# Optimization experiments

Measured on AMD Instinct MI355X. Metric: run time of the kernel, lower is better.

Reference implementation:

```python
import jax, jax.numpy as jnp
import numpy as np

B, S, HID = 1, 4096, 1024
HQ, HKV, D = 16, 4, 64   # query heads, kv heads (GQA), dim_per_head
ROPE_BASE = 10000.0


def setup_inputs() -> dict:
    key = jax.random.key(0)
    ks = jax.random.split(key, 5)
    s = 0.02
    return {
        "x": jax.random.normal(ks[0], (B, S, HID), jnp.float32),
        "Wq": jax.random.normal(ks[1], (HID, HQ * D), jnp.float32) * s,
        "Wk": jax.random.normal(ks[2], (HID, HKV * D), jnp.float32) * s,
        "Wv": jax.random.normal(ks[3], (HID, HKV * D), jnp.float32) * s,
        "Wo": jax.random.normal(ks[4], (HQ * D, HID), jnp.float32) * s,
    }


def _rope(t, cos, sin):
    # non-interleaved (half-split) rotary; t: [B,S,H,D], cos/sin: [S, D//2]
    t1, t2 = jnp.split(t, 2, axis=-1)
    c = cos[None, :, None, :]
    sn = sin[None, :, None, :]
    return jnp.concatenate([t1 * c - t2 * sn, t2 * c + t1 * sn], axis=-1)


def reference(x, Wq, Wk, Wv, Wo):
    # QKV projections (self-attention: key=value=query=x), reshape to [B,S,H,D]
    q = (x @ Wq).reshape(B, S, HQ, D)
    k = (x @ Wk).reshape(B, S, HKV, D)
    v = (x @ Wv).reshape(B, S, HKV, D)

    # rotary position embedding over full head dim
    inv_freq = 1.0 / (ROPE_BASE ** (jnp.arange(0, D, 2, dtype=jnp.float32) / D))
    ang = jnp.arange(S, dtype=jnp.float32)[:, None] * inv_freq[None, :]  # [S, D//2]
    cos, sin = jnp.cos(ang), jnp.sin(ang)
    q = _rope(q, cos, sin)
    k = _rope(k, cos, sin)

    # GQA: expand kv heads to match query heads
    g = HQ // HKV
    k = jnp.repeat(k, g, axis=2)
    v = jnp.repeat(v, g, axis=2)

    scale = D ** -0.5  # attn_scaling ** -0.5 with attn_scaling = dim_per_head
    scores = jnp.einsum('bqhd,bkhd->bhqk', q, k) * scale  # [B,HQ,S,S]
    causal = jnp.tril(jnp.ones((S, S), dtype=bool))
    scores = jnp.where(causal[None, None], scores, jnp.finfo(scores.dtype).min)
    attn = jax.nn.softmax(scores, axis=-1)

    ctx = jnp.einsum('bhqk,bkhd->bqhd', attn, v).reshape(B, S, HQ * D)
    return ctx @ Wo
```

## Files before the change

### kernel.cpp

```cpp
#include <hip/hip_runtime.h>
#include <hip/hip_bf16.h>
#include <math.h>

typedef __attribute__((ext_vector_type(8))) short short8;
typedef __attribute__((ext_vector_type(4))) float f32x4;

#define S_   4096
#define HQ_  16
#define HKV_ 4
#define D_   64

static __device__ __forceinline__ unsigned short f2b(float f) {
    __hip_bfloat16 h = __float2bfloat16(f);
    return *reinterpret_cast<unsigned short*>(&h);
}
static __device__ __forceinline__ float b2f(unsigned short u) {
    union { unsigned int u; float f; } c;
    c.u = ((unsigned int)u) << 16;
    return c.f;
}

typedef __attribute__((address_space(1))) const unsigned int gas_u32;
typedef __attribute__((address_space(3))) unsigned int las_u32;
static __device__ __forceinline__ void gload16(const void* g, void* l) {
    __builtin_amdgcn_global_load_lds((gas_u32*)g, (las_u32*)l, 16, 0, 0);
}


__global__ __launch_bounds__(256) void k_prep(const float* __restrict__ Wq,
                                              const float* __restrict__ Wk,
                                              const float* __restrict__ Wv,
                                              const float* __restrict__ Wo,
                                              const float* __restrict__ x,
                                              unsigned short* __restrict__ WT,
                                              unsigned short* __restrict__ WoT,
                                              unsigned short* __restrict__ xb,
                                              float* __restrict__ cs) {
    const int z = blockIdx.z;
    const int t = threadIdx.x;
    if (z == 4) {
        int flat = blockIdx.y * 32 + blockIdx.x;
#pragma unroll
        for (int ii = 0; ii < 4; ++ii) {
            int i = flat * 1024 + ii * 256 + t;
            float4 v = ((const float4*)x)[i];
            ushort4 o;
            o.x = f2b(v.x); o.y = f2b(v.y); o.z = f2b(v.z); o.w = f2b(v.w);
            ((ushort4*)xb)[i] = o;
        }
        return;
    }
    if (z == 5) {
        int flat = blockIdx.y * 32 + blockIdx.x;
        if (flat >= 512) return;
        int i = flat * 256 + t;
        int s = i >> 5, jj = i & 31;
        float invf = exp2f(-(float)jj * (13.287712379549449f / 32.0f));
        float ang = (float)s * invf;
        ((float2*)cs)[i] = make_float2(cosf(ang), sinf(ang));
        return;
    }
    const float* tin; unsigned short* tout; int N, gx;
    if (z == 0)      { tin = Wq; tout = WT;                 N = 1024; gx = 32; }
    else if (z == 1) { tin = Wk; tout = WT + 1024 * 1024;   N = 256;  gx = 8;  }
    else if (z == 2) { tin = Wv; tout = WT + 1280 * 1024;   N = 256;  gx = 8;  }
    else             { tin = Wo; tout = WoT;                N = 1024; gx = 32; }
    if ((int)blockIdx.x >= gx) return;
    __shared__ float tile[32][33];
    int tx = t & 31, ty = t >> 5;
    int n0 = blockIdx.x * 32, k0 = blockIdx.y * 32;
#pragma unroll
    for (int r = 0; r < 32; r += 8)
        tile[ty + r][tx] = tin[(size_t)(k0 + ty + r) * N + n0 + tx];
    __syncthreads();
#pragma unroll
    for (int r = 0; r < 32; r += 8)
        tout[(size_t)(n0 + ty + r) * 1024 + k0 + tx] = f2b(tile[tx][ty + r]);
}


__global__ __launch_bounds__(256, 3)
void k_gemm_qkv(const unsigned short* __restrict__ A,
                const unsigned short* __restrict__ BT,
                const float* __restrict__ cs,
                unsigned short* __restrict__ Qr,
                unsigned short* __restrict__ Kr,
                unsigned short* __restrict__ Vt) {
    __shared__ unsigned short As[128 * 128];
    __shared__ unsigned short Bs[64 * 128];
    const int t = threadIdx.x;
    const int ntile = blockIdx.x;
    const int n0 = ntile * 64;
    const int m0 = blockIdx.y * 128;
    const int w = t >> 6, lane = t & 63, lr = lane & 15, lg = lane >> 4;
    const int srr = w * 4 + (lane >> 4);
    const int sby = (lane & 15) * 16;
    const int K = 1024;

    f32x4 acc[2][4];
#pragma unroll
    for (int m = 0; m < 2; ++m)
#pragma unroll
        for (int n = 0; n < 4; ++n) acc[m][n] = (f32x4){0.f, 0.f, 0.f, 0.f};

    for (int k0 = 0; k0 < K; k0 += 128) {
#pragma unroll
        for (int c = 0; c < 8; ++c) {
            int r = c * 16 + srr;
            gload16((const char*)&A[(size_t)(m0 + r) * K + k0] + (sby ^ ((r & 7) << 4)),
                    (char*)As + c * 4096 + w * 1024);
        }
#pragma unroll
        for (int c = 0; c < 4; ++c) {
            int r = c * 16 + srr;
            gload16((const char*)&BT[(size_t)(n0 + r) * K + k0] + (sby ^ ((r & 7) << 4)),
                    (char*)Bs + c * 4096 + w * 1024);
        }
        __syncthreads();
#pragma unroll
        for (int kk = 0; kk < 4; ++kk) {
            short8 af[2], bf[4];
#pragma unroll
            for (int m = 0; m < 2; ++m) {
                int arow = w * 32 + m * 16 + lr;
                af[m] = *(const short8*)((const char*)As + arow * 256 +
                                         ((kk * 64 + lg * 16) ^ ((arow & 7) << 4)));
            }
#pragma unroll
            for (int n = 0; n < 4; ++n) {
                int brow = n * 16 + lr;
                bf[n] = *(const short8*)((const char*)Bs + brow * 256 +
                                         ((kk * 64 + lg * 16) ^ ((brow & 7) << 4)));
            }
#pragma unroll
            for (int m = 0; m < 2; ++m)
#pragma unroll
                for (int n = 0; n < 4; ++n)
                    acc[m][n] = __builtin_amdgcn_mfma_f32_16x16x32_bf16(af[m], bf[n], acc[m][n], 0, 0, 0);
        }
        __syncthreads();
    }

    if (ntile < 20) {
        const float QS = (ntile < 16) ? 0.125f * 1.44269504088896340736f : 1.0f;
        unsigned short* dst = (ntile < 16) ? (Qr + (size_t)ntile * (S_ * D_))
                                           : (Kr + (size_t)(ntile - 16) * (S_ * D_));
#pragma unroll
        for (int m = 0; m < 2; ++m)
#pragma unroll
            for (int rr = 0; rr < 4; ++rr) {
                int s = m0 + w * 32 + m * 16 + lg * 4 + rr;
                const float2* csr = (const float2*)cs + s * 32;
                float2 c0 = csr[lr];
                float2 c1 = csr[16 + lr];
                float t1 = acc[m][0][rr], t2 = acc[m][2][rr];
                dst[(size_t)s * 64 + lr]      = f2b((t1 * c0.x - t2 * c0.y) * QS);
                dst[(size_t)s * 64 + 32 + lr] = f2b((t2 * c0.x + t1 * c0.y) * QS);
                t1 = acc[m][1][rr]; t2 = acc[m][3][rr];
                dst[(size_t)s * 64 + 16 + lr] = f2b((t1 * c1.x - t2 * c1.y) * QS);
                dst[(size_t)s * 64 + 48 + lr] = f2b((t2 * c1.x + t1 * c1.y) * QS);
            }
    } else {
        int h2 = ntile - 20;
        unsigned short* dst = Vt + (size_t)h2 * (D_ * S_);
#pragma unroll
        for (int m = 0; m < 2; ++m)
#pragma unroll
            for (int n = 0; n < 4; ++n)
#pragma unroll
                for (int rr = 0; rr < 4; ++rr) {
                    int s = m0 + w * 32 + m * 16 + lg * 4 + rr;
                    dst[(size_t)(n * 16 + lr) * S_ + s] = f2b(acc[m][n][rr]);
                }
    }
}


__global__ __launch_bounds__(256, 3)
void k_gemm_o(const unsigned short* __restrict__ A,
              const unsigned short* __restrict__ BT,
              float* __restrict__ out) {
    __shared__ unsigned short As[128 * 128];
    __shared__ unsigned short Bs[64 * 128];
    const int t = threadIdx.x;
    const int n0 = blockIdx.x * 64;
    const int m0 = blockIdx.y * 128;
    const int w = t >> 6, lane = t & 63, lr = lane & 15, lg = lane >> 4;
    const int srr = w * 4 + (lane >> 4);
    const int sby = (lane & 15) * 16;
    const int K = 1024;

    f32x4 acc[2][4];
#pragma unroll
    for (int m = 0; m < 2; ++m)
#pragma unroll
        for (int n = 0; n < 4; ++n) acc[m][n] = (f32x4){0.f, 0.f, 0.f, 0.f};

    for (int k0 = 0; k0 < K; k0 += 128) {
#pragma unroll
        for (int c = 0; c < 8; ++c) {
            int r = c * 16 + srr;
            gload16((const char*)&A[(size_t)(m0 + r) * K + k0] + (sby ^ ((r & 7) << 4)),
                    (char*)As + c * 4096 + w * 1024);
        }
#pragma unroll
        for (int c = 0; c < 4; ++c) {
            int r = c * 16 + srr;
            gload16((const char*)&BT[(size_t)(n0 + r) * K + k0] + (sby ^ ((r & 7) << 4)),
                    (char*)Bs + c * 4096 + w * 1024);
        }
        __syncthreads();
#pragma unroll
        for (int kk = 0; kk < 4; ++kk) {
            short8 af[2], bf[4];
#pragma unroll
            for (int m = 0; m < 2; ++m) {
                int arow = w * 32 + m * 16 + lr;
                af[m] = *(const short8*)((const char*)As + arow * 256 +
                                         ((kk * 64 + lg * 16) ^ ((arow & 7) << 4)));
            }
#pragma unroll
            for (int n = 0; n < 4; ++n) {
                int brow = n * 16 + lr;
                bf[n] = *(const short8*)((const char*)Bs + brow * 256 +
                                         ((kk * 64 + lg * 16) ^ ((brow & 7) << 4)));
            }
#pragma unroll
            for (int m = 0; m < 2; ++m)
#pragma unroll
                for (int n = 0; n < 4; ++n)
                    acc[m][n] = __builtin_amdgcn_mfma_f32_16x16x32_bf16(af[m], bf[n], acc[m][n], 0, 0, 0);
        }
        __syncthreads();
    }
#pragma unroll
    for (int m = 0; m < 2; ++m)
#pragma unroll
        for (int n = 0; n < 4; ++n)
#pragma unroll
            for (int rr = 0; rr < 4; ++rr) {
                int row = m0 + w * 32 + m * 16 + lg * 4 + rr;
                int col = n0 + n * 16 + lr;
                out[(size_t)row * 1024 + col] = acc[m][n][rr];
            }
}


__global__ __launch_bounds__(256, 4)
void k_attn(const unsigned short* __restrict__ Qr,
            const unsigned short* __restrict__ Kr,
            const unsigned short* __restrict__ Vt,
            unsigned short* __restrict__ Pacc,
            float* __restrict__ Psv) {
    __shared__ unsigned short Ks[2][64 * 64];
    __shared__ unsigned short Vs[2][64 * 64];

    const int t = threadIdx.x;
    const int p = blockIdx.x;
    const int h = blockIdx.y;
    const int j = blockIdx.z;
    const int kvh = h >> 2;
    const int w = t >> 6, lane = t & 63, lr = lane & 15, lg = lane >> 4;

    const unsigned short* Qh = Qr + (size_t)h * (S_ * D_);
    const unsigned short* Kh = Kr + (size_t)kvh * (S_ * D_);
    const unsigned short* Vh = Vt + (size_t)kvh * (D_ * S_);

    const int xw = (lr & 7) << 4;
    const int sr = lane >> 3, sch = (lane & 7) * 16;
    const int r0a = w * 16, r0b = w * 16 + 8;

#pragma unroll 1
    for (int half = 0; half < 2; ++half) {
        const int qb = half ? p : (63 - p);
        const int tend = qb + 1;
        const int qi = qb * 64 + w * 16 + lr;

        const char* kp[2];
        const char* vp[2];
        {
            int ra = r0a + sr, rb = r0b + sr;
            kp[0] = (const char*)(Kh + (size_t)(j * 64 + ra) * 64) + (sch ^ ((ra & 7) << 4));
            kp[1] = (const char*)(Kh + (size_t)(j * 64 + rb) * 64) + (sch ^ ((rb & 7) << 4));
            vp[0] = (const char*)(Vh + (size_t)ra * S_ + j * 64) + (sch ^ ((ra & 7) << 4));
            vp[1] = (const char*)(Vh + (size_t)rb * S_ + j * 64) + (sch ^ ((rb & 7) << 4));
        }
        auto stage = [&](int buf) {
            gload16(kp[0], (char*)&Ks[buf][0] + r0a * 128);
            gload16(kp[1], (char*)&Ks[buf][0] + r0b * 128);
            gload16(vp[0], (char*)&Vs[buf][0] + r0a * 128);
            gload16(vp[1], (char*)&Vs[buf][0] + r0b * 128);
            kp[0] += 16384; kp[1] += 16384;
            vp[0] += 256;   vp[1] += 256;
        };

        short8 aq[2];
        {
            int qrow = qb * 64 + w * 16 + lr;
            aq[0] = *(const short8*)&Qh[(size_t)qrow * 64 + lg * 8];
            aq[1] = *(const short8*)&Qh[(size_t)qrow * 64 + 32 + lg * 8];
        }
        float svl = 0.f;
        f32x4 acc_o[4];
#pragma unroll
        for (int i = 0; i < 4; ++i) acc_o[i] = (f32x4){0.f, 0.f, 0.f, 0.f};

        int cur = 0;
        stage(0);
        __syncthreads();

        for (int kb = j; kb < tend; kb += 2) {
            if (kb + 2 < tend) stage(cur ^ 1);

            f32x4 s[4];
#pragma unroll
            for (int i = 0; i < 4; ++i) s[i] = (f32x4){0.f, 0.f, 0.f, 0.f};
            const char* KsB = (const char*)&Ks[cur][0];
            __builtin_amdgcn_s_setprio(1);
#pragma unroll
            for (int kk = 0; kk < 2; ++kk)
#pragma unroll
                for (int nt = 0; nt < 4; ++nt) {
                    int brow = nt * 16 + lr;
                    short8 kf = *(const short8*)(KsB + brow * 128 + ((kk * 64 + lg * 16) ^ xw));
                    s[nt] = __builtin_amdgcn_mfma_f32_16x16x32_bf16(kf, aq[kk], s[nt], 0, 0, 0);
                }
            __builtin_amdgcn_s_setprio(0);

            if (kb == qb) {
                int kbase = kb * 64 + lg * 4;
#pragma unroll
                for (int nt = 0; nt < 4; ++nt)
#pragma unroll
                    for (int rr = 0; rr < 4; ++rr)
                        if (kbase + nt * 16 + rr > qi) s[nt][rr] = -INFINITY;
            }

            unsigned int wd[8];
#pragma unroll
            for (int nt = 0; nt < 4; ++nt) {
                float p0 = exp2f(s[nt][0]), p1 = exp2f(s[nt][1]);
                float p2 = exp2f(s[nt][2]), p3 = exp2f(s[nt][3]);
                svl += (p0 + p1) + (p2 + p3);
                asm("v_cvt_pk_bf16_f32 %0, %1, %2" : "=v"(wd[nt * 2])     : "v"(p0), "v"(p1));
                asm("v_cvt_pk_bf16_f32 %0, %1, %2" : "=v"(wd[nt * 2 + 1]) : "v"(p2), "v"(p3));
            }

            const char* VsB = (const char*)&Vs[cur][0];
            __builtin_amdgcn_s_setprio(1);
#pragma unroll
            for (int kk = 0; kk < 2; ++kk) {
                union { unsigned int u[4]; short8 s8; } pa;
                pa.u[0] = wd[4 * kk + 0]; pa.u[1] = wd[4 * kk + 1];
                pa.u[2] = wd[4 * kk + 2]; pa.u[3] = wd[4 * kk + 3];
#pragma unroll
                for (int nt = 0; nt < 4; ++nt) {
                    int drow = nt * 16 + lr;
                    union { unsigned long long q[2]; short8 s8; } vb;
                    vb.q[0] = *(const unsigned long long*)(VsB + drow * 128 +
                              ((kk * 64 + lg * 8) ^ xw));
                    vb.q[1] = *(const unsigned long long*)(VsB + drow * 128 +
                              ((kk * 64 + 32 + lg * 8) ^ xw));
                    acc_o[nt] = __builtin_amdgcn_mfma_f32_16x16x32_bf16(pa.s8, vb.s8, acc_o[nt], 0, 0, 0);
                }
            }
            __builtin_amdgcn_s_setprio(0);

            __syncthreads();
            cur ^= 1;
        }

        svl += __shfl_xor(svl, 16);
        svl += __shfl_xor(svl, 32);
        const int u = ((j * 64 + qb) * 16 + h);
        if (lg == 0) Psv[u * 64 + w * 16 + lr] = svl;
        unsigned short* Pb = Pacc + (size_t)u * 4096;
#pragma unroll
        for (int nt = 0; nt < 4; ++nt) {
            int rr = w * 16 + lg * 4;
            int col = nt * 16 + lr;
            Pb[(rr + 0) * 64 + col] = f2b(acc_o[nt][0]);
            Pb[(rr + 1) * 64 + col] = f2b(acc_o[nt][1]);
            Pb[(rr + 2) * 64 + col] = f2b(acc_o[nt][2]);
            Pb[(rr + 3) * 64 + col] = f2b(acc_o[nt][3]);
        }
    }
}


__global__ __launch_bounds__(256) void k_combine(const unsigned short* __restrict__ Pacc,
                                                 const float* __restrict__ Psv,
                                                 unsigned short* __restrict__ O) {
    const int qb = blockIdx.x, h = blockIdx.y;
    const int t = threadIdx.x;
    const int r = t >> 2, db = (t & 3) * 16;
    const int u0 = (qb * 16 + h);
    const int u1 = ((64 + qb) * 16 + h);
    float sa = Psv[u0 * 64 + r], sb = Psv[u1 * 64 + r];
    float inv = 1.f / (sa + sb);
    const unsigned short* A_ = Pacc + (size_t)u0 * 4096 + r * 64 + db;
    const unsigned short* B_ = Pacc + (size_t)u1 * 4096 + r * 64 + db;
    unsigned short* Op = O + (size_t)(qb * 64 + r) * 1024 + h * 64 + db;
#pragma unroll
    for (int halfv = 0; halfv < 2; ++halfv) {
        short8 va = *(const short8*)(A_ + halfv * 8);
        short8 vb = *(const short8*)(B_ + halfv * 8);
        short8 o;
#pragma unroll
        for (int i = 0; i < 8; ++i)
            o[i] = (short)f2b((b2f((unsigned short)va[i]) + b2f((unsigned short)vb[i])) * inv);
        *(short8*)(Op + halfv * 8) = o;
    }
}


extern "C" void kernel_launch(void* const* d_in, const int* in_sizes, int n_in,
                              void* d_out, int out_size, void* d_ws, size_t ws_size,
                              hipStream_t stream) {
    const float* x  = (const float*)d_in[0];
    const float* Wq = (const float*)d_in[1];
    const float* Wk = (const float*)d_in[2];
    const float* Wv = (const float*)d_in[3];
    const float* Wo = (const float*)d_in[4];
    float* out = (float*)d_out;
    char* ws = (char*)d_ws;

    unsigned short* WT  = (unsigned short*)(ws + 0);
    unsigned short* WoT = (unsigned short*)(ws + 3145728);
    unsigned short* Qr  = (unsigned short*)(ws + 5242880);
    unsigned short* Kr  = (unsigned short*)(ws + 13631488);
    unsigned short* Vt  = (unsigned short*)(ws + 15728640);
    unsigned short* O   = (unsigned short*)(ws + 17825792);
    float* cs           = (float*)(ws + 26214400);
    unsigned short* xb  = (unsigned short*)(ws + 27262976);
    unsigned short* Pacc = (unsigned short*)(ws + 27262976);
    float* Psv           = (float*)(ws + 44040192);

    k_prep<<<dim3(32, 32, 6), 256, 0, stream>>>(Wq, Wk, Wv, Wo, x, WT, WoT, xb, cs);
    k_gemm_qkv<<<dim3(24, 32), 256, 0, stream>>>(xb, WT, cs, Qr, Kr, Vt);
    k_attn<<<dim3(32, 16, 2), 256, 0, stream>>>(Qr, Kr, Vt, Pacc, Psv);
    k_combine<<<dim3(64, 16), 256, 0, stream>>>(Pacc, Psv, O);
    k_gemm_o<<<dim3(16, 32), 256, 0, stream>>>(O, WoT, out);
}
```

Measured before the change: 120.6 us.

## Process 128 query rows per attention block and permute V layout for vector loads

The attention kernel now handles a 128-row query tile per block, with each wave owning two 16-row MFMA fragments. Each K/V tile staged in shared memory therefore feeds twice as many MFMAs, and the earlier two-half load-balancing loop is replaced by reverse block ordering. The V store in the QKV GEMM writes a permuted position order as 4-wide vector stores, so the attention PV step can read V fragments with a single 16-byte load instead of two 8-byte loads. This costs more registers per wave, which may lower occupancy under the four-blocks launch bound, and it coarsens the causal-diagonal work per block.

```diff
diff --git a/kernel.cpp b/kernel.cpp
--- a/kernel.cpp
+++ b/kernel.cpp
@@ -85,7 +85,7 @@
                 const float* __restrict__ cs,
                 unsigned short* __restrict__ Qr,
                 unsigned short* __restrict__ Kr,
-                unsigned short* __restrict__ Vt) {
+                unsigned short* __restrict__ Vp) {
     __shared__ unsigned short As[128 * 128];
     __shared__ unsigned short Bs[64 * 128];
     const int t = threadIdx.x;
@@ -162,16 +162,18 @@
             }
     } else {
         int h2 = ntile - 20;
-        unsigned short* dst = Vt + (size_t)h2 * (D_ * S_);
+        unsigned short* dst = Vp + (size_t)h2 * (D_ * S_);
 #pragma unroll
         for (int m = 0; m < 2; ++m)
 #pragma unroll
-            for (int n = 0; n < 4; ++n)
-#pragma unroll
-                for (int rr = 0; rr < 4; ++rr) {
-                    int s = m0 + w * 32 + m * 16 + lg * 4 + rr;
-                    dst[(size_t)(n * 16 + lr) * S_ + s] = f2b(acc[m][n][rr]);
-                }
+            for (int n = 0; n < 4; ++n) {
+                int d = n * 16 + lr;
+                int pos = m0 + (w >> 1) * 64 + (w & 1) * 32 + lg * 8 + m * 4;
+                ushort4 o;
+                o.x = f2b(acc[m][n][0]); o.y = f2b(acc[m][n][1]);
+                o.z = f2b(acc[m][n][2]); o.w = f2b(acc[m][n][3]);
+                *(ushort4*)&dst[(size_t)d * S_ + pos] = o;
+            }
     }
 }
 
@@ -249,14 +251,14 @@
 __global__ __launch_bounds__(256, 4)
 void k_attn(const unsigned short* __restrict__ Qr,
             const unsigned short* __restrict__ Kr,
-            const unsigned short* __restrict__ Vt,
+            const unsigned short* __restrict__ Vp,
             unsigned short* __restrict__ Pacc,
             float* __restrict__ Psv) {
     __shared__ unsigned short Ks[2][64 * 64];
     __shared__ unsigned short Vs[2][64 * 64];
 
     const int t = threadIdx.x;
-    const int p = blockIdx.x;
+    const int qb = 31 - (int)blockIdx.x;
     const int h = blockIdx.y;
     const int j = blockIdx.z;
     const int kvh = h >> 2;
@@ -264,143 +266,152 @@
 
     const unsigned short* Qh = Qr + (size_t)h * (S_ * D_);
     const unsigned short* Kh = Kr + (size_t)kvh * (S_ * D_);
-    const unsigned short* Vh = Vt + (size_t)kvh * (D_ * S_);
+    const unsigned short* Vh = Vp + (size_t)kvh * (D_ * S_);
 
     const int xw = (lr & 7) << 4;
     const int sr = lane >> 3, sch = (lane & 7) * 16;
     const int r0a = w * 16, r0b = w * 16 + 8;
 
-#pragma unroll 1
-    for (int half = 0; half < 2; ++half) {
-        const int qb = half ? p : (63 - p);
-        const int tend = qb + 1;
-        const int qi = qb * 64 + w * 16 + lr;
-
-        const char* kp[2];
-        const char* vp[2];
-        {
-            int ra = r0a + sr, rb = r0b + sr;
-            kp[0] = (const char*)(Kh + (size_t)(j * 64 + ra) * 64) + (sch ^ ((ra & 7) << 4));
-            kp[1] = (const char*)(Kh + (size_t)(j * 64 + rb) * 64) + (sch ^ ((rb & 7) << 4));
-            vp[0] = (const char*)(Vh + (size_t)ra * S_ + j * 64) + (sch ^ ((ra & 7) << 4));
-            vp[1] = (const char*)(Vh + (size_t)rb * S_ + j * 64) + (sch ^ ((rb & 7) << 4));
-        }
-        auto stage = [&](int buf) {
-            gload16(kp[0], (char*)&Ks[buf][0] + r0a * 128);
-            gload16(kp[1], (char*)&Ks[buf][0] + r0b * 128);
-            gload16(vp[0], (char*)&Vs[buf][0] + r0a * 128);
-            gload16(vp[1], (char*)&Vs[buf][0] + r0b * 128);
-            kp[0] += 16384; kp[1] += 16384;
-            vp[0] += 256;   vp[1] += 256;
-        };
-
-        short8 aq[2];
-        {
-            int qrow = qb * 64 + w * 16 + lr;
-            aq[0] = *(const short8*)&Qh[(size_t)qrow * 64 + lg * 8];
-            aq[1] = *(const short8*)&Qh[(size_t)qrow * 64 + 32 + lg * 8];
-        }
-        float svl = 0.f;
-        f32x4 acc_o[4];
-#pragma unroll
-        for (int i = 0; i < 4; ++i) acc_o[i] = (f32x4){0.f, 0.f, 0.f, 0.f};
-
-        int cur = 0;
-        stage(0);
+    const char* kp[2];
+    const char* vp[2];
+    {
+        int ra = r0a + sr, rb = r0b + sr;
+        kp[0] = (const char*)(Kh + (size_t)(j * 64 + ra) * 64) + (sch ^ ((ra & 7) << 4));
+        kp[1] = (const char*)(Kh + (size_t)(j * 64 + rb) * 64) + (sch ^ ((rb & 7) << 4));
+        vp[0] = (const char*)(Vh + (size_t)ra * S_ + j * 64) + (sch ^ ((ra & 7) << 4));
+        vp[1] = (const char*)(Vh + (size_t)rb * S_ + j * 64) + (sch ^ ((rb & 7) << 4));
+    }
+    auto stage = [&](int buf) {
+        gload16(kp[0], (char*)&Ks[buf][0] + r0a * 128);
+        gload16(kp[1], (char*)&Ks[buf][0] + r0b * 128);
+        gload16(vp[0], (char*)&Vs[buf][0] + r0a * 128);
+        gload16(vp[1], (char*)&Vs[buf][0] + r0b * 128);
+        kp[0] += 16384; kp[1] += 16384;
+        vp[0] += 256;   vp[1] += 256;
+    };
+
+    const int qi0 = qb * 128 + w * 32 + lr;
+    short8 aq0[2], aq1[2];
+    {
+        int q0 = qi0;
+        aq0[0] = *(const short8*)&Qh[(size_t)q0 * 64 + lg * 8];
+        aq0[1] = *(const short8*)&Qh[(size_t)q0 * 64 + 32 + lg * 8];
+        aq1[0] = *(const short8*)&Qh[(size_t)(q0 + 16) * 64 + lg * 8];
+        aq1[1] = *(const short8*)&Qh[(size_t)(q0 + 16) * 64 + 32 + lg * 8];
+    }
+    float svl0 = 0.f, svl1 = 0.f;
+    f32x4 acc0[4], acc1[4];
+#pragma unroll
+    for (int i = 0; i < 4; ++i) { acc0[i] = (f32x4){0.f,0.f,0.f,0.f}; acc1[i] = (f32x4){0.f,0.f,0.f,0.f}; }
+
+    const int lastkb = 2 * qb + 1;
+    int cur = 0;
+    stage(0);
+    __syncthreads();
+
+    for (int kb = j; kb <= lastkb; kb += 2) {
+        if (kb + 2 <= lastkb) stage(cur ^ 1);
+
+        f32x4 s0[4], s1[4];
+#pragma unroll
+        for (int i = 0; i < 4; ++i) { s0[i] = (f32x4){0.f,0.f,0.f,0.f}; s1[i] = (f32x4){0.f,0.f,0.f,0.f}; }
+        const char* KsB = (const char*)&Ks[cur][0];
+        __builtin_amdgcn_s_setprio(1);
+#pragma unroll
+        for (int kk = 0; kk < 2; ++kk)
+#pragma unroll
+            for (int nt = 0; nt < 4; ++nt) {
+                short8 kf = *(const short8*)(KsB + (nt * 16 + lr) * 128 + ((kk * 64 + lg * 16) ^ xw));
+                s0[nt] = __builtin_amdgcn_mfma_f32_16x16x32_bf16(kf, aq0[kk], s0[nt], 0, 0, 0);
+                s1[nt] = __builtin_amdgcn_mfma_f32_16x16x32_bf16(kf, aq1[kk], s1[nt], 0, 0, 0);
+            }
+        __builtin_amdgcn_s_setprio(0);
+
+        if (kb >= 2 * qb) {
+            int kbase = kb * 64 + lg * 4;
+#pragma unroll
+            for (int nt = 0; nt < 4; ++nt)
+#pragma unroll
+                for (int rr = 0; rr < 4; ++rr) {
+                    int ki = kbase + nt * 16 + rr;
+                    if (ki > qi0) s0[nt][rr] = -INFINITY;
+                    if (ki > qi0 + 16) s1[nt][rr] = -INFINITY;
+                }
+        }
+
+        unsigned int wd0[8], wd1[8];
+#pragma unroll
+        for (int nt = 0; nt < 4; ++nt) {
+            float p0 = exp2f(s0[nt][0]), p1 = exp2f(s0[nt][1]);
+            float p2 = exp2f(s0[nt][2]), p3 = exp2f(s0[nt][3]);
+            svl0 += (p0 + p1) + (p2 + p3);
+            asm("v_cvt_pk_bf16_f32 %0, %1, %2" : "=v"(wd0[nt * 2])     : "v"(p0), "v"(p1));
+            asm("v_cvt_pk_bf16_f32 %0, %1, %2" : "=v"(wd0[nt * 2 + 1]) : "v"(p2), "v"(p3));
+        }
+#pragma unroll
+        for (int nt = 0; nt < 4; ++nt) {
+            float p0 = exp2f(s1[nt][0]), p1 = exp2f(s1[nt][1]);
+            float p2 = exp2f(s1[nt][2]), p3 = exp2f(s1[nt][3]);
+            svl1 += (p0 + p1) + (p2 + p3);
+            asm("v_cvt_pk_bf16_f32 %0, %1, %2" : "=v"(wd1[nt * 2])     : "v"(p0), "v"(p1));
+            asm("v_cvt_pk_bf16_f32 %0, %1, %2" : "=v"(wd1[nt * 2 + 1]) : "v"(p2), "v"(p3));
+        }
+
+        const char* VsB = (const char*)&Vs[cur][0];
+        __builtin_amdgcn_s_setprio(1);
+#pragma unroll
+        for (int kk = 0; kk < 2; ++kk) {
+            union { unsigned int u[4]; short8 s8; } pa0, pa1;
+#pragma unroll
+            for (int q = 0; q < 4; ++q) { pa0.u[q] = wd0[4 * kk + q]; pa1.u[q] = wd1[4 * kk + q]; }
+#pragma unroll
+            for (int nt = 0; nt < 4; ++nt) {
+                short8 vb = *(const short8*)(VsB + (nt * 16 + lr) * 128 + ((kk * 64 + lg * 16) ^ xw));
+                acc0[nt] = __builtin_amdgcn_mfma_f32_16x16x32_bf16(pa0.s8, vb, acc0[nt], 0, 0, 0);
+                acc1[nt] = __builtin_amdgcn_mfma_f32_16x16x32_bf16(pa1.s8, vb, acc1[nt], 0, 0, 0);
+            }
+        }
+        __builtin_amdgcn_s_setprio(0);
+
         __syncthreads();
-
-        for (int kb = j; kb < tend; kb += 2) {
-            if (kb + 2 < tend) stage(cur ^ 1);
-
-            f32x4 s[4];
-#pragma unroll
-            for (int i = 0; i < 4; ++i) s[i] = (f32x4){0.f, 0.f, 0.f, 0.f};
-            const char* KsB = (const char*)&Ks[cur][0];
-            __builtin_amdgcn_s_setprio(1);
-#pragma unroll
-            for (int kk = 0; kk < 2; ++kk)
-#pragma unroll
-                for (int nt = 0; nt < 4; ++nt) {
-                    int brow = nt * 16 + lr;
-                    short8 kf = *(const short8*)(KsB + brow * 128 + ((kk * 64 + lg * 16) ^ xw));
-                    s[nt] = __builtin_amdgcn_mfma_f32_16x16x32_bf16(kf, aq[kk], s[nt], 0, 0, 0);
-                }
-            __builtin_amdgcn_s_setprio(0);
-
-            if (kb == qb) {
-                int kbase = kb * 64 + lg * 4;
-#pragma unroll
-                for (int nt = 0; nt < 4; ++nt)
-#pragma unroll
-                    for (int rr = 0; rr < 4; ++rr)
-                        if (kbase + nt * 16 + rr > qi) s[nt][rr] = -INFINITY;
-            }
-
-            unsigned int wd[8];
-#pragma unroll
-            for (int nt = 0; nt < 4; ++nt) {
-                float p0 = exp2f(s[nt][0]), p1 = exp2f(s[nt][1]);
-                float p2 = exp2f(s[nt][2]), p3 = exp2f(s[nt][3]);
-                svl += (p0 + p1) + (p2 + p3);
-                asm("v_cvt_pk_bf16_f32 %0, %1, %2" : "=v"(wd[nt * 2])     : "v"(p0), "v"(p1));
-                asm("v_cvt_pk_bf16_f32 %0, %1, %2" : "=v"(wd[nt * 2 + 1]) : "v"(p2), "v"(p3));
-            }
-
-            const char* VsB = (const char*)&Vs[cur][0];
-            __builtin_amdgcn_s_setprio(1);
-#pragma unroll
-            for (int kk = 0; kk < 2; ++kk) {
-                union { unsigned int u[4]; short8 s8; } pa;
-                pa.u[0] = wd[4 * kk + 0]; pa.u[1] = wd[4 * kk + 1];
-                pa.u[2] = wd[4 * kk + 2]; pa.u[3] = wd[4 * kk + 3];
-#pragma unroll
-                for (int nt = 0; nt < 4; ++nt) {
-                    int drow = nt * 16 + lr;
-                    union { unsigned long long q[2]; short8 s8; } vb;
-                    vb.q[0] = *(const unsigned long long*)(VsB + drow * 128 +
-                              ((kk * 64 + lg * 8) ^ xw));
-                    vb.q[1] = *(const unsigned long long*)(VsB + drow * 128 +
-                              ((kk * 64 + 32 + lg * 8) ^ xw));
-                    acc_o[nt] = __builtin_amdgcn_mfma_f32_16x16x32_bf16(pa.s8, vb.s8, acc_o[nt], 0, 0, 0);
-                }
-            }
-            __builtin_amdgcn_s_setprio(0);
-
-            __syncthreads();
-            cur ^= 1;
-        }
-
-        svl += __shfl_xor(svl, 16);
-        svl += __shfl_xor(svl, 32);
-        const int u = ((j * 64 + qb) * 16 + h);
-        if (lg == 0) Psv[u * 64 + w * 16 + lr] = svl;
-        unsigned short* Pb = Pacc + (size_t)u * 4096;
-#pragma unroll
-        for (int nt = 0; nt < 4; ++nt) {
-            int rr = w * 16 + lg * 4;
+        cur ^= 1;
+    }
+
+    svl0 += __shfl_xor(svl0, 16); svl0 += __shfl_xor(svl0, 32);
+    svl1 += __shfl_xor(svl1, 16); svl1 += __shfl_xor(svl1, 32);
+    const int u = (j * 32 + qb) * 16 + h;
+    if (lg == 0) {
+        Psv[u * 128 + w * 32 + lr] = svl0;
+        Psv[u * 128 + w * 32 + 16 + lr] = svl1;
+    }
+    unsigned short* Pb = Pacc + (size_t)u * 8192;
+#pragma unroll
+    for (int nt = 0; nt < 4; ++nt)
+#pragma unroll
+        for (int rr = 0; rr < 4; ++rr) {
+            int row0 = w * 32 + lg * 4 + rr;
             int col = nt * 16 + lr;
-            Pb[(rr + 0) * 64 + col] = f2b(acc_o[nt][0]);
-            Pb[(rr + 1) * 64 + col] = f2b(acc_o[nt][1]);
-            Pb[(rr + 2) * 64 + col] = f2b(acc_o[nt][2]);
-            Pb[(rr + 3) * 64 + col] = f2b(acc_o[nt][3]);
-        }
-    }
+            Pb[row0 * 64 + col] = f2b(acc0[nt][rr]);
+            Pb[(row0 + 16) * 64 + col] = f2b(acc1[nt][rr]);
+        }
 }
 
 
 __global__ __launch_bounds__(256) void k_combine(const unsigned short* __restrict__ Pacc,
                                                  const float* __restrict__ Psv,
                                                  unsigned short* __restrict__ O) {
-    const int qb = blockIdx.x, h = blockIdx.y;
+    const int qb64 = blockIdx.x, h = blockIdx.y;
     const int t = threadIdx.x;
     const int r = t >> 2, db = (t & 3) * 16;
-    const int u0 = (qb * 16 + h);
-    const int u1 = ((64 + qb) * 16 + h);
-    float sa = Psv[u0 * 64 + r], sb = Psv[u1 * 64 + r];
+    const int qb128 = qb64 >> 1;
+    const int rloc = (qb64 & 1) * 64 + r;
+    const int u0 = qb128 * 16 + h;
+    const int u1 = (32 + qb128) * 16 + h;
+    float sa = Psv[u0 * 128 + rloc], sb = Psv[u1 * 128 + rloc];
     float inv = 1.f / (sa + sb);
-    const unsigned short* A_ = Pacc + (size_t)u0 * 4096 + r * 64 + db;
-    const unsigned short* B_ = Pacc + (size_t)u1 * 4096 + r * 64 + db;
-    unsigned short* Op = O + (size_t)(qb * 64 + r) * 1024 + h * 64 + db;
+    const unsigned short* A_ = Pacc + (size_t)u0 * 8192 + rloc * 64 + db;
+    const unsigned short* B_ = Pacc + (size_t)u1 * 8192 + rloc * 64 + db;
+    unsigned short* Op = O + (size_t)(qb64 * 64 + r) * 1024 + h * 64 + db;
 #pragma unroll
     for (int halfv = 0; halfv < 2; ++halfv) {
         short8 va = *(const short8*)(A_ + halfv * 8);
@@ -429,7 +440,7 @@
     unsigned short* WoT = (unsigned short*)(ws + 3145728);
     unsigned short* Qr  = (unsigned short*)(ws + 5242880);
     unsigned short* Kr  = (unsigned short*)(ws + 13631488);
-    unsigned short* Vt  = (unsigned short*)(ws + 15728640);
+    unsigned short* Vp  = (unsigned short*)(ws + 15728640);
     unsigned short* O   = (unsigned short*)(ws + 17825792);
     float* cs           = (float*)(ws + 26214400);
     unsigned short* xb  = (unsigned short*)(ws + 27262976);
@@ -437,8 +448,8 @@
     float* Psv           = (float*)(ws + 44040192);
 
     k_prep<<<dim3(32, 32, 6), 256, 0, stream>>>(Wq, Wk, Wv, Wo, x, WT, WoT, xb, cs);
-    k_gemm_qkv<<<dim3(24, 32), 256, 0, stream>>>(xb, WT, cs, Qr, Kr, Vt);
-    k_attn<<<dim3(32, 16, 2), 256, 0, stream>>>(Qr, Kr, Vt, Pacc, Psv);
+    k_gemm_qkv<<<dim3(24, 32), 256, 0, stream>>>(xb, WT, cs, Qr, Kr, Vp);
+    k_attn<<<dim3(32, 16, 2), 256, 0, stream>>>(Qr, Kr, Vp, Pacc, Psv);
     k_combine<<<dim3(64, 16), 256, 0, stream>>>(Pacc, Psv, O);
     k_gemm_o<<<dim3(16, 32), 256, 0, stream>>>(O, WoT, out);
 }
```

Measured after the change: 150.5 us. 1.25x slower.

## Permute V sequence layout so attention PV reads use single 16-byte LDS loads

Applied to the files above, without the earlier changes.

The QKV GEMM now writes transposed V with a permuted sequence order inside each 64-position block and stores four contiguous bf16 values per write instead of scalar stores. The attention kernel matches this permutation, so each lane's V fragment for the PV MFMA comes from one 16-byte LDS read instead of two 8-byte reads. This reduces LDS instruction count in the inner loop and makes the V stores wider. It relies on the permutation being consistent with the P fragment ordering and with the K-dimension reduction being order-invariant.

```diff
diff --git a/kernel.cpp b/kernel.cpp
--- a/kernel.cpp
+++ b/kernel.cpp
@@ -85,7 +85,7 @@
                 const float* __restrict__ cs,
                 unsigned short* __restrict__ Qr,
                 unsigned short* __restrict__ Kr,
-                unsigned short* __restrict__ Vt) {
+                unsigned short* __restrict__ Vp) {
     __shared__ unsigned short As[128 * 128];
     __shared__ unsigned short Bs[64 * 128];
     const int t = threadIdx.x;
@@ -162,16 +162,18 @@
             }
     } else {
         int h2 = ntile - 20;
-        unsigned short* dst = Vt + (size_t)h2 * (D_ * S_);
+        unsigned short* dst = Vp + (size_t)h2 * (D_ * S_);
 #pragma unroll
         for (int m = 0; m < 2; ++m)
 #pragma unroll
-            for (int n = 0; n < 4; ++n)
-#pragma unroll
-                for (int rr = 0; rr < 4; ++rr) {
-                    int s = m0 + w * 32 + m * 16 + lg * 4 + rr;
-                    dst[(size_t)(n * 16 + lr) * S_ + s] = f2b(acc[m][n][rr]);
-                }
+            for (int n = 0; n < 4; ++n) {
+                int d = n * 16 + lr;
+                int pos = m0 + (w >> 1) * 64 + (w & 1) * 32 + lg * 8 + m * 4;
+                ushort4 o;
+                o.x = f2b(acc[m][n][0]); o.y = f2b(acc[m][n][1]);
+                o.z = f2b(acc[m][n][2]); o.w = f2b(acc[m][n][3]);
+                *(ushort4*)&dst[(size_t)d * S_ + pos] = o;
+            }
     }
 }
 
@@ -249,7 +251,7 @@
 __global__ __launch_bounds__(256, 4)
 void k_attn(const unsigned short* __restrict__ Qr,
             const unsigned short* __restrict__ Kr,
-            const unsigned short* __restrict__ Vt,
+            const unsigned short* __restrict__ Vp,
             unsigned short* __restrict__ Pacc,
             float* __restrict__ Psv) {
     __shared__ unsigned short Ks[2][64 * 64];
@@ -264,7 +266,7 @@
 
     const unsigned short* Qh = Qr + (size_t)h * (S_ * D_);
     const unsigned short* Kh = Kr + (size_t)kvh * (S_ * D_);
-    const unsigned short* Vh = Vt + (size_t)kvh * (D_ * S_);
+    const unsigned short* Vh = Vp + (size_t)kvh * (D_ * S_);
 
     const int xw = (lr & 7) << 4;
     const int sr = lane >> 3, sch = (lane & 7) * 16;
@@ -321,8 +323,7 @@
             for (int kk = 0; kk < 2; ++kk)
 #pragma unroll
                 for (int nt = 0; nt < 4; ++nt) {
-                    int brow = nt * 16 + lr;
-                    short8 kf = *(const short8*)(KsB + brow * 128 + ((kk * 64 + lg * 16) ^ xw));
+                    short8 kf = *(const short8*)(KsB + (nt * 16 + lr) * 128 + ((kk * 64 + lg * 16) ^ xw));
                     s[nt] = __builtin_amdgcn_mfma_f32_16x16x32_bf16(kf, aq[kk], s[nt], 0, 0, 0);
                 }
             __builtin_amdgcn_s_setprio(0);
@@ -355,13 +356,8 @@
                 pa.u[2] = wd[4 * kk + 2]; pa.u[3] = wd[4 * kk + 3];
 #pragma unroll
                 for (int nt = 0; nt < 4; ++nt) {
-                    int drow = nt * 16 + lr;
-                    union { unsigned long long q[2]; short8 s8; } vb;
-                    vb.q[0] = *(const unsigned long long*)(VsB + drow * 128 +
-                              ((kk * 64 + lg * 8) ^ xw));
-                    vb.q[1] = *(const unsigned long long*)(VsB + drow * 128 +
-                              ((kk * 64 + 32 + lg * 8) ^ xw));
-                    acc_o[nt] = __builtin_amdgcn_mfma_f32_16x16x32_bf16(pa.s8, vb.s8, acc_o[nt], 0, 0, 0);
+                    short8 vb = *(const short8*)(VsB + (nt * 16 + lr) * 128 + ((kk * 64 + lg * 16) ^ xw));
+                    acc_o[nt] = __builtin_amdgcn_mfma_f32_16x16x32_bf16(pa.s8, vb, acc_o[nt], 0, 0, 0);
                 }
             }
             __builtin_amdgcn_s_setprio(0);
@@ -429,7 +425,7 @@
     unsigned short* WoT = (unsigned short*)(ws + 3145728);
     unsigned short* Qr  = (unsigned short*)(ws + 5242880);
     unsigned short* Kr  = (unsigned short*)(ws + 13631488);
-    unsigned short* Vt  = (unsigned short*)(ws + 15728640);
+    unsigned short* Vp  = (unsigned short*)(ws + 15728640);
     unsigned short* O   = (unsigned short*)(ws + 17825792);
     float* cs           = (float*)(ws + 26214400);
     unsigned short* xb  = (unsigned short*)(ws + 27262976);
@@ -437,8 +433,8 @@
     float* Psv           = (float*)(ws + 44040192);
 
     k_prep<<<dim3(32, 32, 6), 256, 0, stream>>>(Wq, Wk, Wv, Wo, x, WT, WoT, xb, cs);
-    k_gemm_qkv<<<dim3(24, 32), 256, 0, stream>>>(xb, WT, cs, Qr, Kr, Vt);
-    k_attn<<<dim3(32, 16, 2), 256, 0, stream>>>(Qr, Kr, Vt, Pacc, Psv);
+    k_gemm_qkv<<<dim3(24, 32), 256, 0, stream>>>(xb, WT, cs, Qr, Kr, Vp);
+    k_attn<<<dim3(32, 16, 2), 256, 0, stream>>>(Qr, Kr, Vp, Pacc, Psv);
     k_combine<<<dim3(64, 16), 256, 0, stream>>>(Pacc, Psv, O);
     k_gemm_o<<<dim3(16, 32), 256, 0, stream>>>(O, WoT, out);
 }
```

Result: faster. 116.6 us (-3.3%).
